# Kernel optimization log

Hardware: AMD Instinct MI355X
Metric: run time of the kernel (lower is better)

Reference implementation:

```python
import jax, jax.numpy as jnp
import numpy as np

B, S, I, H = 64, 512, 1024, 1024

def setup_inputs() -> dict:
    key = jax.random.key(0)
    ks = jax.random.split(key, 5)
    sqrt_k = 1.0 / np.sqrt(H)
    return {
        "sequence": jax.random.normal(ks[0], (B, S, I), dtype=jnp.float32),
        "hidden_state": jnp.zeros((B, H), dtype=jnp.float32),
        "w_ih": jax.random.uniform(ks[1], (H, I), dtype=jnp.float32, minval=-sqrt_k, maxval=sqrt_k),
        "w_hh": jax.random.uniform(ks[2], (H, H), dtype=jnp.float32, minval=-sqrt_k, maxval=sqrt_k),
        "b_ih": jax.random.uniform(ks[3], (H,), dtype=jnp.float32, minval=-sqrt_k, maxval=sqrt_k),
        "b_hh": jax.random.uniform(ks[4], (H,), dtype=jnp.float32, minval=-sqrt_k, maxval=sqrt_k),
    }

def reference(sequence, hidden_state, w_ih, w_hh, b_ih, b_hh):
    # Precompute the input projection for all timesteps in one big GEMM:
    # x_proj[b,s,h] = sequence[b,s,:] @ w_ih.T + b_ih
    x_proj = jnp.einsum('bsi,hi->bsh', sequence, w_ih) + b_ih

    def step(h, x_t):
        # h_new = relu(x_t + h @ w_hh.T + b_hh)  -- Elman recurrence
        h_new = jax.nn.relu(x_t + jnp.einsum('bh,gh->bg', h, w_hh) + b_hh)
        return h_new, h_new

    # scan over time (leading axis)
    h_last, outs = jax.lax.scan(step, hidden_state, jnp.swapaxes(x_proj, 0, 1))
    output = jnp.swapaxes(outs, 0, 1)  # [B, S, H]
    return output, h_last
```

## Files before the change

### kernel.cpp

```cpp
#include <hip/hip_runtime.h>
#include <hip/hip_bf16.h>

#define B_SZ  64
#define S_LEN 512
#define I_DIM 1024
#define H_DIM 1024
#define BH    (B_SZ * H_DIM)

typedef __bf16 bf16x8 __attribute__((ext_vector_type(8)));
typedef __bf16 bf16x4 __attribute__((ext_vector_type(4)));
typedef float  f32x4  __attribute__((ext_vector_type(4)));
typedef unsigned u32x4 __attribute__((ext_vector_type(4)));

#define MFMA16(a,b,c) __builtin_amdgcn_mfma_f32_16x16x32_bf16((a),(b),(c),0,0,0)

__device__ inline bf16x8 cvt8(const float4& a, const float4& b) {
  bf16x8 v;
  v[0]=(__bf16)a.x; v[1]=(__bf16)a.y; v[2]=(__bf16)a.z; v[3]=(__bf16)a.w;
  v[4]=(__bf16)b.x; v[5]=(__bf16)b.y; v[6]=(__bf16)b.z; v[7]=(__bf16)b.w;
  return v;
}
__device__ inline bf16x8 cvt8v(const f32x4& a, const f32x4& b) {
  bf16x8 v;
  v[0]=(__bf16)a[0]; v[1]=(__bf16)a[1]; v[2]=(__bf16)a[2]; v[3]=(__bf16)a[3];
  v[4]=(__bf16)b[0]; v[5]=(__bf16)b[1]; v[6]=(__bf16)b[2]; v[7]=(__bf16)b[3];
  return v;
}

__device__ inline u32x4 load_b128_sc(const void* p) {
  u32x4 r;
  asm volatile("global_load_dwordx4 %0, %1, off sc0 sc1"
               : "=v"(r) : "v"(p) : "memory");
  return r;
}
__device__ inline void st64_sc(void* p, unsigned long long v) {
  asm volatile("global_store_dwordx2 %0, %1, off sc0 sc1"
               :: "v"(p), "v"(v) : "memory");
}
__device__ inline f32x4 load_b128_pf(const void* p) {
  f32x4 r;
  asm volatile("global_load_dwordx4 %0, %1, off"
               : "=v"(r) : "v"(p) : "memory");
  return r;
}
__device__ inline void waitcnt_vm0() {
  asm volatile("s_waitcnt vmcnt(0)" ::: "memory");
}

__global__ void k_hinit(const float* __restrict__ h0, __bf16* __restrict__ ht,
                        unsigned* __restrict__ flags) {
  const int ci = blockIdx.x * 256 + threadIdx.x;
  const float4 v = ((const float4*)h0)[ci];
  bf16x4 hv;
  hv[0] = (__bf16)v.x; hv[1] = (__bf16)v.y; hv[2] = (__bf16)v.z; hv[3] = (__bf16)v.w;
  st64_sc(ht + (size_t)ci * 4, __builtin_bit_cast(unsigned long long, hv));
  if (blockIdx.x == 0) {
    unsigned z = 0u;
    asm volatile("global_store_dword %0, %1, off sc0 sc1"
                 :: "v"(flags + threadIdx.x), "v"(z) : "memory");
  }
}

#define P1_LDA 40
__global__ __launch_bounds__(256, 2) void k_xproj(
    const float* __restrict__ A, const float* __restrict__ W,
    const float* __restrict__ bias, float* __restrict__ C) {
  constexpr int K = I_DIM, N = H_DIM;
  __shared__ __bf16 As[128][P1_LDA];
  __shared__ __bf16 Bs[128][P1_LDA];
  const int bid = blockIdx.x;
  const int nt = bid & 7, mt = bid >> 3;
  const int m0 = mt * 128, n0 = nt * 128;
  const int tid = threadIdx.x, lane = tid & 63, wv = tid >> 6;
  const int wm = (wv & 1) * 64, wn = (wv >> 1) * 64;
  const int fr = lane & 15, fq = lane >> 4;
  const int srow = tid >> 1, scol = (tid & 1) * 16;
  const float* gA = A + (size_t)(m0 + srow) * K + scol;
  const float* gB = W + (size_t)(n0 + srow) * K + scol;
  const f32x4 zero = {0.f, 0.f, 0.f, 0.f};
  f32x4 acc[4][4];
  #pragma unroll
  for (int m = 0; m < 4; ++m)
    #pragma unroll
    for (int n = 0; n < 4; ++n) acc[m][n] = zero;

  for (int k0 = 0; k0 < K; k0 += 32) {
    float4 a0 = *(const float4*)(gA + k0);
    float4 a1 = *(const float4*)(gA + k0 + 4);
    float4 a2 = *(const float4*)(gA + k0 + 8);
    float4 a3 = *(const float4*)(gA + k0 + 12);
    float4 b0 = *(const float4*)(gB + k0);
    float4 b1 = *(const float4*)(gB + k0 + 4);
    float4 b2 = *(const float4*)(gB + k0 + 8);
    float4 b3 = *(const float4*)(gB + k0 + 12);
    __syncthreads();
    *(bf16x8*)(&As[srow][scol])     = cvt8(a0, a1);
    *(bf16x8*)(&As[srow][scol + 8]) = cvt8(a2, a3);
    *(bf16x8*)(&Bs[srow][scol])     = cvt8(b0, b1);
    *(bf16x8*)(&Bs[srow][scol + 8]) = cvt8(b2, b3);
    __syncthreads();
    bf16x8 af[4], bfr[4];
    #pragma unroll
    for (int m = 0; m < 4; ++m) af[m]  = *(const bf16x8*)(&As[wm + m*16 + fr][fq*8]);
    #pragma unroll
    for (int n = 0; n < 4; ++n) bfr[n] = *(const bf16x8*)(&Bs[wn + n*16 + fr][fq*8]);
    #pragma unroll
    for (int m = 0; m < 4; ++m)
      #pragma unroll
      for (int n = 0; n < 4; ++n)
        acc[m][n] = MFMA16(af[m], bfr[n], acc[m][n]);
  }
  #pragma unroll
  for (int n = 0; n < 4; ++n) {
    const int col = n0 + wn + n*16 + fr;
    const float bv = bias[col];
    #pragma unroll
    for (int m = 0; m < 4; ++m) {
      const int row = m0 + wm + m*16 + fq*4;
      #pragma unroll
      for (int jj = 0; jj < 4; ++jj)
        C[(size_t)(row + jj) * N + col] = acc[m][n][jj] + bv;
    }
  }
}

#define NGR 4
#define BG  16
#define WPG 8

__global__ __launch_bounds__(512, 1) void k_rnn(
    const float* __restrict__ w_hh, const float* __restrict__ b_hh,
    float* __restrict__ out, __bf16* __restrict__ ht,
    unsigned* __restrict__ flags)
{
  __shared__ __bf16 Hs[BG][H_DIM];
  const int bid = blockIdx.x;
  const int g = bid >> 3, j = bid & 7;
  const int r0 = j * 128;
  const int tid = threadIdx.x, lane = tid & 63, wv = tid >> 6;
  const int fr = lane & 15, fq = lane >> 4;
  const int myW  = r0 + wv * 16 + fr;
  const int row4 = r0 + wv * 16 + fq * 4;
  const int b    = g * BG + fr;
  const int hswz = (fr & 7) << 3;

  bf16x8 wfrag[32];
  {
    const float* wsrc = w_hh + (size_t)myW * H_DIM + fq * 8;
    #pragma unroll
    for (int kk = 0; kk < 32; ++kk) {
      f32x4 w0 = *(const f32x4*)(wsrc + kk * 32);
      f32x4 w1 = *(const f32x4*)(wsrc + kk * 32 + 4);
      wfrag[kk] = cvt8v(w0, w1);
    }
  }
  const f32x4 bh = *(const f32x4*)(b_hh + row4);
  const size_t bsh = (size_t)B_SZ * S_LEN * H_DIM;
  const __bf16* hg0 = ht + (size_t)g * BG * H_DIM;
  const unsigned* fp = flags + (g << 6) + lane;
  unsigned* myfp = flags + (g << 6) + (j << 3) + wv;

  size_t xo = (size_t)b * S_LEN * H_DIM + row4;
  f32x4 xv = load_b128_pf(out + xo);

  for (int t = 0; t < S_LEN; ++t) {
    if (t) {
      const unsigned tt = (unsigned)t;
      for (;;) {
        unsigned f;
        asm volatile("global_load_dword %0, %1, off sc0 sc1"
                     : "=v"(f) : "v"(fp) : "memory");
        waitcnt_vm0();
        __builtin_amdgcn_sched_barrier(0);
        if (__all((int)(f >= tt))) break;
      }
    }

    const __bf16* hsrc = hg0 + (size_t)(t & 1) * BH;
    u32x4 st[4];
    #pragma unroll
    for (int i = 0; i < 4; ++i)
      st[i] = load_b128_sc(hsrc + (size_t)(tid + (i << 9)) * 8);
    waitcnt_vm0();
    __builtin_amdgcn_sched_barrier(0);
    #pragma unroll
    for (int i = 0; i < 4; ++i) {
      const int c = tid + (i << 9);
      const int bb = c >> 7, k = (c & 127) << 3;
      *(u32x4*)&Hs[bb][k ^ ((bb & 7) << 3)] = st[i];
    }
    __syncthreads();

    const f32x4 z = {0.f, 0.f, 0.f, 0.f};
    f32x4 a0 = z, a1 = z, a2 = z, a3 = z;
    #pragma unroll
    for (int kk = 0; kk < 32; kk += 4) {
      bf16x8 h0 = *(const bf16x8*)&Hs[fr][((kk + 0) * 32 + fq * 8) ^ hswz];
      a0 = MFMA16(wfrag[kk + 0], h0, a0);
      bf16x8 h1 = *(const bf16x8*)&Hs[fr][((kk + 1) * 32 + fq * 8) ^ hswz];
      a1 = MFMA16(wfrag[kk + 1], h1, a1);
      bf16x8 h2 = *(const bf16x8*)&Hs[fr][((kk + 2) * 32 + fq * 8) ^ hswz];
      a2 = MFMA16(wfrag[kk + 2], h2, a2);
      bf16x8 h3 = *(const bf16x8*)&Hs[fr][((kk + 3) * 32 + fq * 8) ^ hswz];
      a3 = MFMA16(wfrag[kk + 3], h3, a3);
    }

    f32x4 s = (a0 + a1) + (a2 + a3);
    f32x4 r;
    r[0] = fmaxf(xv[0] + s[0] + bh[0], 0.f);
    r[1] = fmaxf(xv[1] + s[1] + bh[1], 0.f);
    r[2] = fmaxf(xv[2] + s[2] + bh[2], 0.f);
    r[3] = fmaxf(xv[3] + s[3] + bh[3], 0.f);
    *(f32x4*)(out + xo) = r;
    if (t == S_LEN - 1)
      *(f32x4*)(out + bsh + (size_t)b * H_DIM + row4) = r;
    bf16x4 hv;
    hv[0] = (__bf16)r[0]; hv[1] = (__bf16)r[1];
    hv[2] = (__bf16)r[2]; hv[3] = (__bf16)r[3];
    __bf16* hd = ht + (size_t)((t + 1) & 1) * BH + (size_t)b * H_DIM + row4;
    st64_sc(hd, __builtin_bit_cast(unsigned long long, hv));

    waitcnt_vm0();
    if (lane == 0) {
      unsigned tv = (unsigned)(t + 1);
      asm volatile("global_store_dword %0, %1, off sc0 sc1"
                   :: "v"(myfp), "v"(tv) : "memory");
    }
    xo += H_DIM;
    xv = load_b128_pf(out + xo);
    __syncthreads();
  }
}

extern "C" void kernel_launch(void* const* d_in, const int* in_sizes, int n_in,
                              void* d_out, int out_size, void* d_ws, size_t ws_size,
                              hipStream_t stream) {
  const float* seq  = (const float*)d_in[0];
  const float* h0   = (const float*)d_in[1];
  const float* w_ih = (const float*)d_in[2];
  const float* w_hh = (const float*)d_in[3];
  const float* b_ih = (const float*)d_in[4];
  const float* b_hh = (const float*)d_in[5];
  float* out = (float*)d_out;

  __bf16* ht = (__bf16*)d_ws;
  unsigned* flags = (unsigned*)((char*)d_ws + (size_t)2 * BH * sizeof(__bf16));

  k_hinit<<<dim3(BH / 4 / 256), dim3(256), 0, stream>>>(h0, ht, flags);
  k_xproj<<<dim3((B_SZ * S_LEN / 128) * (H_DIM / 128)), dim3(256), 0, stream>>>(
      seq, w_ih, b_ih, out);

  const float* a0 = w_hh; const float* a1 = b_hh; float* a2 = out;
  __bf16* a3 = ht; unsigned* a4 = flags;
  void* args[5] = { &a0, &a1, &a2, &a3, &a4 };
  hipLaunchCooperativeKernel((void*)k_rnn, dim3(NGR * WPG), dim3(512),
                             args, 0, stream);
}
```

Measured before the change: 1.964 ms.

## Split recurrence across 64 workgroups of 4 waves and signal flags earlier

The recurrent kernel now runs 16 workgroups per batch group, each with 4 waves covering 64 hidden rows, instead of 8 workgroups of 8 waves covering 128 rows. This spreads the per-step matvec over more CUs and cuts per-block work, at the cost of more flag polling and each block loading the full hidden state. The hidden-state store and flag publish also move ahead of the fp32 output store, with the barrier placed right after the MFMA loop, so consumers are unblocked sooner on the critical path.

```diff
diff --git a/kernel.cpp b/kernel.cpp
--- a/kernel.cpp
+++ b/kernel.cpp
@@ -5,7 +5,7 @@
 #define S_LEN 512
 #define I_DIM 1024
 #define H_DIM 1024
-#define BH    (B_SZ * H_DIM)
+#define BHE   (B_SZ * H_DIM)
 
 typedef __bf16 bf16x8 __attribute__((ext_vector_type(8)));
 typedef __bf16 bf16x4 __attribute__((ext_vector_type(4)));
@@ -26,6 +26,11 @@
   v[4]=(__bf16)b[0]; v[5]=(__bf16)b[1]; v[6]=(__bf16)b[2]; v[7]=(__bf16)b[3];
   return v;
 }
+__device__ inline unsigned long long pack4(const f32x4& r) {
+  bf16x4 h;
+  h[0]=(__bf16)r[0]; h[1]=(__bf16)r[1]; h[2]=(__bf16)r[2]; h[3]=(__bf16)r[3];
+  return __builtin_bit_cast(unsigned long long, h);
+}
 
 __device__ inline u32x4 load_b128_sc(const void* p) {
   u32x4 r;
@@ -39,8 +44,7 @@
 }
 __device__ inline f32x4 load_b128_pf(const void* p) {
   f32x4 r;
-  asm volatile("global_load_dwordx4 %0, %1, off"
-               : "=v"(r) : "v"(p) : "memory");
+  asm volatile("global_load_dwordx4 %0, %1, off" : "=v"(r) : "v"(p) : "memory");
   return r;
 }
 __device__ inline void waitcnt_vm0() {
@@ -126,17 +130,18 @@
 
 #define NGR 4
 #define BG  16
-#define WPG 8
-
-__global__ __launch_bounds__(512, 1) void k_rnn(
+#define WPG 16
+#define RPW 64
+
+__global__ __launch_bounds__(256, 1) void k_rnn(
     const float* __restrict__ w_hh, const float* __restrict__ b_hh,
     float* __restrict__ out, __bf16* __restrict__ ht,
     unsigned* __restrict__ flags)
 {
   __shared__ __bf16 Hs[BG][H_DIM];
   const int bid = blockIdx.x;
-  const int g = bid >> 3, j = bid & 7;
-  const int r0 = j * 128;
+  const int g = bid >> 4, j = bid & 15;
+  const int r0 = j * RPW;
   const int tid = threadIdx.x, lane = tid & 63, wv = tid >> 6;
   const int fr = lane & 15, fq = lane >> 4;
   const int myW  = r0 + wv * 16 + fr;
@@ -157,8 +162,9 @@
   const f32x4 bh = *(const f32x4*)(b_hh + row4);
   const size_t bsh = (size_t)B_SZ * S_LEN * H_DIM;
   const __bf16* hg0 = ht + (size_t)g * BG * H_DIM;
-  const unsigned* fp = flags + (g << 6) + lane;
-  unsigned* myfp = flags + (g << 6) + (j << 3) + wv;
+  unsigned* fgrp = flags + (g << 6);
+  const unsigned* fpoll = fgrp + ((tid & 127) >> 1);
+  unsigned* myfp = fgrp + (j << 2) + wv;
 
   size_t xo = (size_t)b * S_LEN * H_DIM + row4;
   f32x4 xv = load_b128_pf(out + xo);
@@ -169,23 +175,23 @@
       for (;;) {
         unsigned f;
         asm volatile("global_load_dword %0, %1, off sc0 sc1"
-                     : "=v"(f) : "v"(fp) : "memory");
+                     : "=v"(f) : "v"(fpoll) : "memory");
         waitcnt_vm0();
         __builtin_amdgcn_sched_barrier(0);
         if (__all((int)(f >= tt))) break;
       }
     }
 
-    const __bf16* hsrc = hg0 + (size_t)(t & 1) * BH;
-    u32x4 st[4];
-    #pragma unroll
-    for (int i = 0; i < 4; ++i)
-      st[i] = load_b128_sc(hsrc + (size_t)(tid + (i << 9)) * 8);
+    const __bf16* hsrc = hg0 + (size_t)(t & 1) * BHE;
+    u32x4 st[8];
+    #pragma unroll
+    for (int i = 0; i < 8; ++i)
+      st[i] = load_b128_sc(hsrc + (size_t)(tid + (i << 8)) * 8);
     waitcnt_vm0();
     __builtin_amdgcn_sched_barrier(0);
     #pragma unroll
-    for (int i = 0; i < 4; ++i) {
-      const int c = tid + (i << 9);
+    for (int i = 0; i < 8; ++i) {
+      const int c = tid + (i << 8);
       const int bb = c >> 7, k = (c & 127) << 3;
       *(u32x4*)&Hs[bb][k ^ ((bb & 7) << 3)] = st[i];
     }
@@ -204,6 +210,7 @@
       bf16x8 h3 = *(const bf16x8*)&Hs[fr][((kk + 3) * 32 + fq * 8) ^ hswz];
       a3 = MFMA16(wfrag[kk + 3], h3, a3);
     }
+    __syncthreads();
 
     f32x4 s = (a0 + a1) + (a2 + a3);
     f32x4 r;
@@ -211,24 +218,19 @@
     r[1] = fmaxf(xv[1] + s[1] + bh[1], 0.f);
     r[2] = fmaxf(xv[2] + s[2] + bh[2], 0.f);
     r[3] = fmaxf(xv[3] + s[3] + bh[3], 0.f);
+    __bf16* hd = ht + (size_t)((t + 1) & 1) * BHE + (size_t)b * H_DIM + row4;
+    st64_sc(hd, pack4(r));
+    waitcnt_vm0();
+    if (lane == 0) {
+      const unsigned tv = (unsigned)(t + 1);
+      asm volatile("global_store_dword %0, %1, off sc0 sc1"
+                   :: "v"(myfp), "v"(tv) : "memory");
+    }
     *(f32x4*)(out + xo) = r;
     if (t == S_LEN - 1)
       *(f32x4*)(out + bsh + (size_t)b * H_DIM + row4) = r;
-    bf16x4 hv;
-    hv[0] = (__bf16)r[0]; hv[1] = (__bf16)r[1];
-    hv[2] = (__bf16)r[2]; hv[3] = (__bf16)r[3];
-    __bf16* hd = ht + (size_t)((t + 1) & 1) * BH + (size_t)b * H_DIM + row4;
-    st64_sc(hd, __builtin_bit_cast(unsigned long long, hv));
-
-    waitcnt_vm0();
-    if (lane == 0) {
-      unsigned tv = (unsigned)(t + 1);
-      asm volatile("global_store_dword %0, %1, off sc0 sc1"
-                   :: "v"(myfp), "v"(tv) : "memory");
-    }
     xo += H_DIM;
     xv = load_b128_pf(out + xo);
-    __syncthreads();
   }
 }
 
@@ -244,15 +246,15 @@
   float* out = (float*)d_out;
 
   __bf16* ht = (__bf16*)d_ws;
-  unsigned* flags = (unsigned*)((char*)d_ws + (size_t)2 * BH * sizeof(__bf16));
-
-  k_hinit<<<dim3(BH / 4 / 256), dim3(256), 0, stream>>>(h0, ht, flags);
+  unsigned* flags = (unsigned*)((char*)d_ws + (size_t)2 * BHE * sizeof(__bf16));
+
+  k_hinit<<<dim3(BHE / 4 / 256), dim3(256), 0, stream>>>(h0, ht, flags);
   k_xproj<<<dim3((B_SZ * S_LEN / 128) * (H_DIM / 128)), dim3(256), 0, stream>>>(
       seq, w_ih, b_ih, out);
 
   const float* a0 = w_hh; const float* a1 = b_hh; float* a2 = out;
   __bf16* a3 = ht; unsigned* a4 = flags;
   void* args[5] = { &a0, &a1, &a2, &a3, &a4 };
-  hipLaunchCooperativeKernel((void*)k_rnn, dim3(NGR * WPG), dim3(512),
+  hipLaunchCooperativeKernel((void*)k_rnn, dim3(NGR * WPG), dim3(256),
                              args, 0, stream);
 }
```

After: 2.110 ms. +7.4%, slower.
